# Kernel tuning notes

Hardware: AMD Instinct MI355X
Metric: run time of the kernel (lower is better)

The kernel has to match this reference:

```python
import jax, jax.numpy as jnp
import numpy as np

B, S, D, H = 2, 4096, 512, 8
DK = D // H  # 64

def setup_inputs() -> dict:
    key = jax.random.key(0)
    k1, k2, k3, k4 = jax.random.split(key, 4)
    return {
        "queries": jax.random.normal(k1, (B, S, D), dtype=jnp.float32),
        "keys": jax.random.normal(k2, (B, S, D), dtype=jnp.float32),
        "values": jax.random.normal(k3, (B, S, D), dtype=jnp.float32),
        "W_o": jax.random.normal(k4, (D, D), dtype=jnp.float32) * (1.0 / np.sqrt(D)),
        "b_o": jnp.zeros((D,), dtype=jnp.float32),
    }

def reference(queries, keys, values, W_o, b_o):
    b_s, nq, _ = queries.shape
    nk = keys.shape[1]
    # split heads: (b, s, h, dk) -> (b, h, s, dk)
    q = queries.reshape(b_s, nq, H, DK).transpose(0, 2, 1, 3)
    k = keys.reshape(b_s, nk, H, DK).transpose(0, 2, 1, 3)
    v = values.reshape(b_s, nk, H, DK).transpose(0, 2, 1, 3)
    # full (nq, nk) attention matrix, scaled by sqrt(d_k)
    att = jnp.einsum("bhqd,bhkd->bhqk", q, k) / np.sqrt(DK).astype(np.float32)
    att = jax.nn.softmax(att, axis=-1)  # dropout is identity at inference
    out = jnp.einsum("bhqk,bhkd->bhqd", att, v)
    out = out.transpose(0, 2, 1, 3).reshape(b_s, nq, H * DK)
    return out @ W_o + b_o
```

## Files before the change

### kernel.cpp

```cpp
#include <hip/hip_runtime.h>
#include <hip/hip_bf16.h>

#define Bn 2
#define Sn 4096
#define Dn 512
#define Hn 8

typedef _Float16 f16x8 __attribute__((ext_vector_type(8)));
typedef __fp16 fp16x2 __attribute__((ext_vector_type(2)));
typedef float f32x16 __attribute__((ext_vector_type(16)));

static __device__ __forceinline__ unsigned pkh(float a, float b) {
    union { fp16x2 h; unsigned u; } r;
    r.h = __builtin_amdgcn_cvt_pkrtz(a, b);
    return r.u;
}

static __device__ __forceinline__ f16x8 xchg2(unsigned g0x, unsigned g0y,
                                              unsigned g1x, unsigned g1y, int hi) {
    int sx = hi ? (int)g0x : (int)g1x;
    int sy = hi ? (int)g0y : (int)g1y;
    int rx = __shfl_xor(sx, 32);
    int ry = __shfl_xor(sy, 32);
    unsigned ox = hi ? g1x : g0x;
    unsigned oy = hi ? g1y : g0y;
    union { unsigned u[4]; f16x8 v; } f;
    f.u[0] = hi ? (unsigned)rx : ox;
    f.u[1] = hi ? (unsigned)ry : oy;
    f.u[2] = hi ? ox : (unsigned)rx;
    f.u[3] = hi ? oy : (unsigned)ry;
    return f.v;
}

__global__ __launch_bounds__(256) void prep_kernel(
    const float* __restrict__ K, const float* __restrict__ V, const float* __restrict__ W,
    unsigned short* __restrict__ Kb, unsigned short* __restrict__ Vb,
    unsigned short* __restrict__ Wb) {
    const int vb = blockIdx.x;
    const int tid = threadIdx.x;
    if (vb < 1024) {
        const int kt = vb & 63, bh = vb >> 6;
        const int b = bh >> 3, h = bh & 7;
        unsigned short* dst = Kb + ((size_t)bh * 64 + kt) * 4096;
#pragma unroll
        for (int i = 0; i < 2; ++i) {
            int c = tid + i * 256;
            int f = c >> 6, ln = c & 63;
            int ktile = f >> 2, ks = f & 3;
            int row = ktile * 32 + (ln & 31);
            int dk = ks * 16 + (ln >> 5) * 8;
            const float* src = K + ((size_t)(b * Sn + kt * 64 + row)) * Dn + h * 64 + dk;
            float4 a0 = *(const float4*)src;
            float4 a1 = *(const float4*)(src + 4);
            uint4 o;
            o.x = pkh(a0.x, a0.y); o.y = pkh(a0.z, a0.w);
            o.z = pkh(a1.x, a1.y); o.w = pkh(a1.z, a1.w);
            *(uint4*)(dst + c * 8) = o;
        }
    } else if (vb < 2048) {
        const int u = vb - 1024;
        const int kt = u & 63, bh = u >> 6;
        const int b = bh >> 3, h = bh & 7;
        unsigned short* dst = Vb + ((size_t)bh * 64 + kt) * 4096;
#pragma unroll
        for (int i = 0; i < 2; ++i) {
            int c = tid + i * 256;
            int f = c >> 6, ln = c & 63;
            int dt = f >> 2, ks = f & 3;
            int dk = dt * 32 + (ln & 31);
            int key0 = ks * 16 + (ln >> 5) * 8;
            const float* src = V + ((size_t)(b * Sn + kt * 64 + key0)) * Dn + h * 64 + dk;
            uint4 o;
            o.x = pkh(src[0 * Dn], src[1 * Dn]);
            o.y = pkh(src[2 * Dn], src[3 * Dn]);
            o.z = pkh(src[4 * Dn], src[5 * Dn]);
            o.w = pkh(src[6 * Dn], src[7 * Dn]);
            *(uint4*)(dst + c * 8) = o;
        }
    } else {
        int c = (vb - 2048) * 256 + tid;
        int ln = c & 63, f = c >> 6;
        int ntile = f >> 5, ks = f & 31;
        int n = ntile * 32 + (ln & 31);
        int k0 = ks * 16 + (ln >> 5) * 8;
        uint4 o;
        o.x = pkh(W[(size_t)(k0 + 0) * Dn + n], W[(size_t)(k0 + 1) * Dn + n]);
        o.y = pkh(W[(size_t)(k0 + 2) * Dn + n], W[(size_t)(k0 + 3) * Dn + n]);
        o.z = pkh(W[(size_t)(k0 + 4) * Dn + n], W[(size_t)(k0 + 5) * Dn + n]);
        o.w = pkh(W[(size_t)(k0 + 6) * Dn + n], W[(size_t)(k0 + 7) * Dn + n]);
        *(uint4*)(Wb + c * 8) = o;
    }
}

__global__ __launch_bounds__(512, 4) void attn_kernel(
    const float* __restrict__ Q,
    const unsigned short* __restrict__ Kb,
    const unsigned short* __restrict__ Vb,
    unsigned short* __restrict__ ObA) {
    __shared__ __align__(16) unsigned short KV[16384];
    __shared__ float Lsh[4][64];

    const int qt = blockIdx.x;
    const int bh = blockIdx.y;
    const int b = bh >> 3, h = bh & 7;
    const int tid = threadIdx.x;
    const int wg = tid >> 6;
    const int half = wg >> 2;
    const int w4 = wg & 3;
    const int lane = tid & 63;
    const int q = lane & 31;
    const int hi = lane >> 5;
    const int q0 = qt * 128 + w4 * 32;
    const int th = tid & 255;
    const float cexp = 0.18033688f;

    unsigned short* Kbuf = KV + half * 4096;
    unsigned short* Vbuf = KV + 8192 + half * 4096;

    f16x8 qf[4];
    {
        const float* qp = Q + ((size_t)(b * Sn + q0 + q)) * Dn + h * 64 + hi * 8;
#pragma unroll
        for (int ks = 0; ks < 4; ++ks) {
            float4 a0 = *(const float4*)(qp + ks * 16);
            float4 a1 = *(const float4*)(qp + ks * 16 + 4);
            union { unsigned u[4]; f16x8 v; } f;
            f.u[0] = pkh(a0.x * cexp, a0.y * cexp);
            f.u[1] = pkh(a0.z * cexp, a0.w * cexp);
            f.u[2] = pkh(a1.x * cexp, a1.y * cexp);
            f.u[3] = pkh(a1.z * cexp, a1.w * cexp);
            qf[ks] = f.v;
        }
    }

    f32x16 zf;
#pragma unroll
    for (int r = 0; r < 16; ++r) zf[r] = 0.f;
    f32x16 oacc[2];
    oacc[0] = zf; oacc[1] = zf;
    float l_ = 0.f;

    const size_t tbase = ((size_t)bh * 64 + half * 32) * 4096;
    const unsigned short* kg = Kb + tbase;
    const unsigned short* vg = Vb + tbase;

    uint4 gk0 = *(const uint4*)(kg + th * 16);
    uint4 gk1 = *(const uint4*)(kg + th * 16 + 8);
    uint4 gv0 = *(const uint4*)(vg + th * 16);
    uint4 gv1 = *(const uint4*)(vg + th * 16 + 8);

    for (int it = 0; it < 32; ++it) {
        __syncthreads();
        *(uint4*)&Kbuf[th * 16] = gk0;
        *(uint4*)&Kbuf[th * 16 + 8] = gk1;
        *(uint4*)&Vbuf[th * 16] = gv0;
        *(uint4*)&Vbuf[th * 16 + 8] = gv1;
        __syncthreads();
        if (it < 31) {
            const unsigned short* ks_ = kg + (size_t)(it + 1) * 4096;
            const unsigned short* vs_ = vg + (size_t)(it + 1) * 4096;
            gk0 = *(const uint4*)(ks_ + th * 16);
            gk1 = *(const uint4*)(ks_ + th * 16 + 8);
            gv0 = *(const uint4*)(vs_ + th * 16);
            gv1 = *(const uint4*)(vs_ + th * 16 + 8);
        }

#pragma unroll
        for (int t = 0; t < 2; ++t) {
            f16x8 ka = *(const f16x8*)&Kbuf[(t * 4 + 0) * 512 + lane * 8];
            f32x16 sa = __builtin_amdgcn_mfma_f32_32x32x16_f16(ka, qf[0], zf, 0, 0, 0);
#pragma unroll
            for (int ks = 1; ks < 4; ++ks) {
                ka = *(const f16x8*)&Kbuf[(t * 4 + ks) * 512 + lane * 8];
                sa = __builtin_amdgcn_mfma_f32_32x32x16_f16(ka, qf[ks], sa, 0, 0, 0);
            }
            float e[16];
            float s0 = 0.f, s1 = 0.f;
#pragma unroll
            for (int r = 0; r < 16; r += 2) {
                e[r] = __builtin_amdgcn_exp2f(sa[r]);
                e[r + 1] = __builtin_amdgcn_exp2f(sa[r + 1]);
                s0 += e[r]; s1 += e[r + 1];
            }
            l_ += s0 + s1;
#pragma unroll
            for (int s2 = 0; s2 < 2; ++s2) {
                unsigned g0x = pkh(e[8 * s2 + 0], e[8 * s2 + 1]);
                unsigned g0y = pkh(e[8 * s2 + 2], e[8 * s2 + 3]);
                unsigned g1x = pkh(e[8 * s2 + 4], e[8 * s2 + 5]);
                unsigned g1y = pkh(e[8 * s2 + 6], e[8 * s2 + 7]);
                f16x8 pb = xchg2(g0x, g0y, g1x, g1y, hi);
                const int kp = t * 2 + s2;
                f16x8 va0 = *(const f16x8*)&Vbuf[(0 * 4 + kp) * 512 + lane * 8];
                f16x8 va1 = *(const f16x8*)&Vbuf[(1 * 4 + kp) * 512 + lane * 8];
                oacc[0] = __builtin_amdgcn_mfma_f32_32x32x16_f16(va0, pb, oacc[0], 0, 0, 0);
                oacc[1] = __builtin_amdgcn_mfma_f32_32x32x16_f16(va1, pb, oacc[1], 0, 0, 0);
            }
        }
    }

    __syncthreads();
    float* rp = (float*)KV + w4 * 2048;
    if (half) {
#pragma unroll
        for (int g = 0; g < 8; ++g) {
            float4 v;
            v.x = oacc[g >> 2][(g & 3) * 4 + 0];
            v.y = oacc[g >> 2][(g & 3) * 4 + 1];
            v.z = oacc[g >> 2][(g & 3) * 4 + 2];
            v.w = oacc[g >> 2][(g & 3) * 4 + 3];
            *(float4*)&rp[g * 256 + lane * 4] = v;
        }
        Lsh[w4][lane] = l_;
    }
    __syncthreads();
    if (!half) {
#pragma unroll
        for (int g = 0; g < 8; ++g) {
            float4 v = *(const float4*)&rp[g * 256 + lane * 4];
            oacc[g >> 2][(g & 3) * 4 + 0] += v.x;
            oacc[g >> 2][(g & 3) * 4 + 1] += v.y;
            oacc[g >> 2][(g & 3) * 4 + 2] += v.z;
            oacc[g >> 2][(g & 3) * 4 + 3] += v.w;
        }
        l_ += Lsh[w4][lane];
        l_ += __shfl_xor(l_, 32);
        const float li = 1.f / l_;
        const int gm = b * 128 + qt * 4 + w4;
#pragma unroll
        for (int ksg = 0; ksg < 4; ++ksg) {
            const int dt = ksg >> 1, k2 = ksg & 1;
            unsigned g0x = pkh(oacc[dt][8 * k2 + 0] * li, oacc[dt][8 * k2 + 1] * li);
            unsigned g0y = pkh(oacc[dt][8 * k2 + 2] * li, oacc[dt][8 * k2 + 3] * li);
            unsigned g1x = pkh(oacc[dt][8 * k2 + 4] * li, oacc[dt][8 * k2 + 5] * li);
            unsigned g1y = pkh(oacc[dt][8 * k2 + 6] * li, oacc[dt][8 * k2 + 7] * li);
            f16x8 frag = xchg2(g0x, g0y, g1x, g1y, hi);
            union { f16x8 v; uint4 u; } fu; fu.v = frag;
            *(uint4*)&ObA[((size_t)(gm * 32 + h * 4 + ksg) * 64 + lane) * 8] = fu.u;
        }
    }
}

__global__ __launch_bounds__(256) void proj_kernel(
    const unsigned short* __restrict__ ObA,
    const unsigned short* __restrict__ Wb,
    const float* __restrict__ bias,
    float* __restrict__ out) {
    __shared__ __align__(16) unsigned short Ash[8192];
    __shared__ __align__(16) unsigned short Wsh[4096];

    const int mt = blockIdx.x;
    const int nt = blockIdx.y;
    const int tid = threadIdx.x;
    const int w = tid >> 6;
    const int lane = tid & 63;
    const int q = lane & 31;
    const int hi = lane >> 5;

    f32x16 acc[2];
#pragma unroll
    for (int t = 0; t < 2; ++t)
#pragma unroll
        for (int r = 0; r < 16; ++r) acc[t][r] = 0.f;

    for (int kt = 0; kt < 8; ++kt) {
        __syncthreads();
#pragma unroll
        for (int i = 0; i < 4; ++i) {
            int ci = (tid >> 6) + i * 4;
            int ml = ci >> 2, ksl = ci & 3;
            *(uint4*)&Ash[ci * 512 + lane * 8] =
                *(const uint4*)(ObA + (((size_t)(mt * 4 + ml) * 32 + kt * 4 + ksl) * 64 + lane) * 8);
        }
#pragma unroll
        for (int i = 0; i < 2; ++i) {
            int ci = (tid >> 6) + i * 4;
            int ntl = ci >> 2, ksl = ci & 3;
            *(uint4*)&Wsh[ci * 512 + lane * 8] =
                *(const uint4*)(Wb + (((size_t)(nt * 2 + ntl) * 32 + kt * 4 + ksl) * 64 + lane) * 8);
        }
        __syncthreads();

#pragma unroll
        for (int ks = 0; ks < 4; ++ks) {
            f16x8 a  = *(const f16x8*)&Ash[(w * 4 + ks) * 512 + lane * 8];
            f16x8 b0 = *(const f16x8*)&Wsh[(0 * 4 + ks) * 512 + lane * 8];
            f16x8 b1 = *(const f16x8*)&Wsh[(4 + ks) * 512 + lane * 8];
            acc[0] = __builtin_amdgcn_mfma_f32_32x32x16_f16(a, b0, acc[0], 0, 0, 0);
            acc[1] = __builtin_amdgcn_mfma_f32_32x32x16_f16(a, b1, acc[1], 0, 0, 0);
        }
    }

#pragma unroll
    for (int ntl = 0; ntl < 2; ++ntl) {
        int col = nt * 64 + ntl * 32 + q;
        float bv = bias[col];
#pragma unroll
        for (int reg = 0; reg < 16; ++reg) {
            int row = mt * 128 + w * 32 + (reg & 3) + 8 * (reg >> 2) + 4 * hi;
            out[(size_t)row * Dn + col] = acc[ntl][reg] + bv;
        }
    }
}

extern "C" void kernel_launch(void* const* d_in, const int* in_sizes, int n_in,
                              void* d_out, int out_size, void* d_ws, size_t ws_size,
                              hipStream_t stream) {
    const float* Q = (const float*)d_in[0];
    const float* K = (const float*)d_in[1];
    const float* V = (const float*)d_in[2];
    const float* W = (const float*)d_in[3];
    const float* bo = (const float*)d_in[4];
    float* out = (float*)d_out;

    char* ws = (char*)d_ws;
    unsigned short* Kb  = (unsigned short*)(ws);
    unsigned short* Vb  = (unsigned short*)(ws + 8388608);
    unsigned short* Wb  = (unsigned short*)(ws + 16777216);
    unsigned short* ObA = (unsigned short*)(ws + 17301504);

    prep_kernel<<<2176, 256, 0, stream>>>(K, V, W, Kb, Vb, Wb);
    attn_kernel<<<dim3(32, 16), 512, 0, stream>>>(Q, Kb, Vb, ObA);
    proj_kernel<<<dim3(64, 8), 256, 0, stream>>>(ObA, Wb, bo, out);
}
```

Before: 189.3 us.

## Double-buffer K/V tiles in LDS and use permlane32_swap for half-wave exchange

Makes the K/V shared-memory staging double-buffered: the next tile is written into the alternate LDS buffer after the compute, which removes one of the two barriers per iteration, and the global prefetch now runs two tiles ahead. It also replaces the shuffle-based half-wave exchange with the permlane32_swap builtin when the compiler provides it, avoiding LDS-routed shuffles and the select instructions. LDS use doubles to 64KB per block, which may reduce occupancy compared with the requested 4 blocks per CU.

```diff
diff --git a/kernel.cpp b/kernel.cpp
--- a/kernel.cpp
+++ b/kernel.cpp
@@ -9,6 +9,7 @@
 typedef _Float16 f16x8 __attribute__((ext_vector_type(8)));
 typedef __fp16 fp16x2 __attribute__((ext_vector_type(2)));
 typedef float f32x16 __attribute__((ext_vector_type(16)));
+typedef unsigned uint2v __attribute__((ext_vector_type(2)));
 
 static __device__ __forceinline__ unsigned pkh(float a, float b) {
     union { fp16x2 h; unsigned u; } r;
@@ -18,17 +19,23 @@
 
 static __device__ __forceinline__ f16x8 xchg2(unsigned g0x, unsigned g0y,
                                               unsigned g1x, unsigned g1y, int hi) {
+    union { unsigned u[4]; f16x8 v; } f;
+#if __has_builtin(__builtin_amdgcn_permlane32_swap)
+    uint2v rx = __builtin_amdgcn_permlane32_swap(g0x, g1x, false, false);
+    uint2v ry = __builtin_amdgcn_permlane32_swap(g0y, g1y, false, false);
+    f.u[0] = rx.x; f.u[1] = ry.x; f.u[2] = rx.y; f.u[3] = ry.y;
+#else
     int sx = hi ? (int)g0x : (int)g1x;
     int sy = hi ? (int)g0y : (int)g1y;
     int rx = __shfl_xor(sx, 32);
     int ry = __shfl_xor(sy, 32);
     unsigned ox = hi ? g1x : g0x;
     unsigned oy = hi ? g1y : g0y;
-    union { unsigned u[4]; f16x8 v; } f;
     f.u[0] = hi ? (unsigned)rx : ox;
     f.u[1] = hi ? (unsigned)ry : oy;
     f.u[2] = hi ? ox : (unsigned)rx;
     f.u[3] = hi ? oy : (unsigned)ry;
+#endif
     return f.v;
 }
 
@@ -97,8 +104,7 @@
     const unsigned short* __restrict__ Kb,
     const unsigned short* __restrict__ Vb,
     unsigned short* __restrict__ ObA) {
-    __shared__ __align__(16) unsigned short KV[16384];
-    __shared__ float Lsh[4][64];
+    __shared__ __align__(16) unsigned short KV[32768];
 
     const int qt = blockIdx.x;
     const int bh = blockIdx.y;
@@ -114,9 +120,6 @@
     const int th = tid & 255;
     const float cexp = 0.18033688f;
 
-    unsigned short* Kbuf = KV + half * 4096;
-    unsigned short* Vbuf = KV + 8192 + half * 4096;
-
     f16x8 qf[4];
     {
         const float* qp = Q + ((size_t)(b * Sn + q0 + q)) * Dn + h * 64 + hi * 8;
@@ -144,26 +147,27 @@
     const unsigned short* kg = Kb + tbase;
     const unsigned short* vg = Vb + tbase;
 
-    uint4 gk0 = *(const uint4*)(kg + th * 16);
-    uint4 gk1 = *(const uint4*)(kg + th * 16 + 8);
-    uint4 gv0 = *(const uint4*)(vg + th * 16);
-    uint4 gv1 = *(const uint4*)(vg + th * 16 + 8);
+    {
+        uint4 a = *(const uint4*)(kg + th * 16);
+        uint4 c = *(const uint4*)(kg + th * 16 + 8);
+        uint4 d = *(const uint4*)(vg + th * 16);
+        uint4 e2 = *(const uint4*)(vg + th * 16 + 8);
+        unsigned short* Kb0 = KV + half * 4096;
+        unsigned short* Vb0 = KV + 8192 + half * 4096;
+        *(uint4*)&Kb0[th * 16] = a;
+        *(uint4*)&Kb0[th * 16 + 8] = c;
+        *(uint4*)&Vb0[th * 16] = d;
+        *(uint4*)&Vb0[th * 16 + 8] = e2;
+    }
+    uint4 gk0 = *(const uint4*)(kg + 4096 + th * 16);
+    uint4 gk1 = *(const uint4*)(kg + 4096 + th * 16 + 8);
+    uint4 gv0 = *(const uint4*)(vg + 4096 + th * 16);
+    uint4 gv1 = *(const uint4*)(vg + 4096 + th * 16 + 8);
 
     for (int it = 0; it < 32; ++it) {
         __syncthreads();
-        *(uint4*)&Kbuf[th * 16] = gk0;
-        *(uint4*)&Kbuf[th * 16 + 8] = gk1;
-        *(uint4*)&Vbuf[th * 16] = gv0;
-        *(uint4*)&Vbuf[th * 16 + 8] = gv1;
-        __syncthreads();
-        if (it < 31) {
-            const unsigned short* ks_ = kg + (size_t)(it + 1) * 4096;
-            const unsigned short* vs_ = vg + (size_t)(it + 1) * 4096;
-            gk0 = *(const uint4*)(ks_ + th * 16);
-            gk1 = *(const uint4*)(ks_ + th * 16 + 8);
-            gv0 = *(const uint4*)(vs_ + th * 16);
-            gv1 = *(const uint4*)(vs_ + th * 16 + 8);
-        }
+        const unsigned short* Kbuf = KV + (it & 1) * 16384 + half * 4096;
+        const unsigned short* Vbuf = KV + (it & 1) * 16384 + 8192 + half * 4096;
 
 #pragma unroll
         for (int t = 0; t < 2; ++t) {
@@ -197,10 +201,28 @@
                 oacc[1] = __builtin_amdgcn_mfma_f32_32x32x16_f16(va1, pb, oacc[1], 0, 0, 0);
             }
         }
+
+        if (it < 31) {
+            unsigned short* nK = KV + ((it + 1) & 1) * 16384 + half * 4096;
+            unsigned short* nV = KV + ((it + 1) & 1) * 16384 + 8192 + half * 4096;
+            *(uint4*)&nK[th * 16] = gk0;
+            *(uint4*)&nK[th * 16 + 8] = gk1;
+            *(uint4*)&nV[th * 16] = gv0;
+            *(uint4*)&nV[th * 16 + 8] = gv1;
+            if (it < 30) {
+                const unsigned short* ks_ = kg + (size_t)(it + 2) * 4096;
+                const unsigned short* vs_ = vg + (size_t)(it + 2) * 4096;
+                gk0 = *(const uint4*)(ks_ + th * 16);
+                gk1 = *(const uint4*)(ks_ + th * 16 + 8);
+                gv0 = *(const uint4*)(vs_ + th * 16);
+                gv1 = *(const uint4*)(vs_ + th * 16 + 8);
+            }
+        }
     }
 
     __syncthreads();
     float* rp = (float*)KV + w4 * 2048;
+    float* Ls = (float*)KV + 8192 + w4 * 64;
     if (half) {
 #pragma unroll
         for (int g = 0; g < 8; ++g) {
@@ -211,7 +233,7 @@
             v.w = oacc[g >> 2][(g & 3) * 4 + 3];
             *(float4*)&rp[g * 256 + lane * 4] = v;
         }
-        Lsh[w4][lane] = l_;
+        Ls[lane] = l_;
     }
     __syncthreads();
     if (!half) {
@@ -223,7 +245,7 @@
             oacc[g >> 2][(g & 3) * 4 + 2] += v.z;
             oacc[g >> 2][(g & 3) * 4 + 3] += v.w;
         }
-        l_ += Lsh[w4][lane];
+        l_ += Ls[lane];
         l_ += __shfl_xor(l_, 32);
         const float li = 1.f / l_;
         const int gm = b * 128 + qt * 4 + w4;
```

New measurement: 185.2 us. 2.2% less time.
